# Kernel tuning notes

Hardware: AMD Instinct MI355X
Metric: run time of the kernel (lower is better)

Reference implementation:

```python
import math
import jax, jax.numpy as jnp
import numpy as np

EMBED_DIM = 128
NUM_HEADS = 2
B, N = 4096, 32  # batch of fully-connected ally graphs, N allies each (self-edges included)


def sparsemax(z, axis):
    """Sparsemax (Martins & Astudillo 2016) along `axis`."""
    K = z.shape[axis]
    z_sorted = -jnp.sort(-z, axis=axis)  # descending
    z_cumsum = jnp.cumsum(z_sorted, axis=axis)
    shape = [1] * z.ndim
    shape[axis] = K
    k = jnp.arange(1, K + 1, dtype=z.dtype).reshape(shape)
    support = (1.0 + k * z_sorted) > z_cumsum
    k_sup = jnp.sum(support.astype(z.dtype), axis=axis, keepdims=True)
    tau = (jnp.sum(jnp.where(support, z_sorted, 0.0), axis=axis, keepdims=True) - 1.0) / k_sup
    return jnp.maximum(z - tau, 0.0)


def setup_inputs() -> dict:
    key = jax.random.key(0)
    k1, k2, k3, k4 = jax.random.split(key, 4)
    D, H = EMBED_DIM, NUM_HEADS
    node_feature = jax.random.normal(k1, (B, N, D), dtype=jnp.float32)
    scale = 1.0 / math.sqrt(D)
    WK = jax.random.normal(k2, (D, H * D), dtype=jnp.float32) * scale
    WV = jax.random.normal(k3, (D, H * D), dtype=jnp.float32) * scale
    WQ = jax.random.normal(k4, (D, H * D), dtype=jnp.float32) * scale
    return {"node_feature": node_feature, "WK": WK, "WV": WV, "WQ": WQ}


def reference(node_feature, WK, WV, WQ):
    D, H = EMBED_DIM, NUM_HEADS
    x = node_feature  # [B, N, D]
    # per-node projections; Linear(D, H*D) reshaped to (H, D) as in torch .view
    k = (x @ WK).reshape(B, N, H, D)
    v = (x @ WV).reshape(B, N, H, D)
    q = (x @ WQ).reshape(B, N, H, D)
    # fully connected graph: node i attends over mailbox of all nodes j in same graph
    score = jnp.einsum("bihd,bjhd->bijh", q, k) / math.sqrt(D * H)  # [B, N(i), N(j), H]
    w = sparsemax(score, axis=2)  # sparsemax over neighbor (mailbox) dim
    out = jnp.einsum("bijh,bjhd->bihd", w, v)  # weighted reduction
    out = out.mean(axis=2)  # mean over heads -> [B, N, D]
    output = out.reshape(B * N, D)
    # weight padded to max_num_allies (= N here, so no extra padding needed)
    weight = w.reshape(B * N, N, H)
    return output, weight
```

## Files before the change

### kernel.cpp

```cpp
#include <hip/hip_runtime.h>
#include <hip/hip_bf16.h>


#define NG 4096

typedef short bf16x8 __attribute__((ext_vector_type(8)));
typedef short bf16x4 __attribute__((ext_vector_type(4)));
typedef float f32x4 __attribute__((ext_vector_type(4)));

__device__ inline short f2bf(float f) {
    __hip_bfloat16 h = __float2bfloat16(f);
    return __builtin_bit_cast(short, h);
}
__device__ inline float bf2f(short s) {
    return __builtin_bit_cast(float, ((unsigned)(unsigned short)s) << 16);
}
__device__ inline unsigned pack2(float a, float b) {
    return (unsigned)(unsigned short)f2bf(a) | ((unsigned)(unsigned short)f2bf(b) << 16);
}

#define TSWZ(node, col) ((((node) << 8)) + (((col) ^ (((node) & 7) << 3))))
#define VSWZ(row, col) ((((row) << 5) + (col)) ^ (((row) & 3) << 3))
#define XSWZ(node, col) (((node) << 7) + (((col) ^ (((node) & 7) << 3))))

__global__ void pack_mv_kernel(const float* __restrict__ WQ, const float* __restrict__ WK,
                               const float* __restrict__ WV,
                               short* __restrict__ pm, short* __restrict__ pv) {
    int gidx = blockIdx.x * 256 + threadIdx.x;
    if (gidx < 32768) {
        int idx  = gidx;
        int jj   = idx & 7;
        int lane = (idx >> 3) & 63;
        int s    = (idx >> 9) & 3;
        int mt   = (idx >> 11) & 15;
        int h    = mt >> 3;
        int a    = s * 32 + (lane >> 4) * 8 + jj;
        int bl   = (mt & 7) * 16 + (lane & 15);
        const float4* qa = (const float4*)(WQ + a * 256 + h * 128);
        const float4* kb = (const float4*)(WK + bl * 256 + h * 128);
        float acc = 0.f;
        #pragma unroll 8
        for (int c = 0; c < 32; ++c) {
            float4 q4 = qa[c], k4 = kb[c];
            acc += q4.x * k4.x + q4.y * k4.y + q4.z * k4.z + q4.w * k4.w;
        }
        pm[idx] = f2bf(acc * 0.0625f);
    } else {
        int idx  = gidx - 32768;
        int jj   = idx & 7;
        int lane = (idx >> 3) & 63;
        int s    = (idx >> 9) & 3;
        int t    = (idx >> 11) & 15;
        int krow = s * 32 + (lane >> 4) * 8 + jj;
        int col  = t * 16 + (lane & 15);
        pv[idx] = f2bf(WV[krow * 256 + col]);
    }
}

__global__ __launch_bounds__(256, 4)
void fused_attn_kernel(const float* __restrict__ x, const short* __restrict__ pm,
                       const short* __restrict__ pv, float* __restrict__ out,
                       float* __restrict__ wgt) {
    __shared__ char __align__(16) smem[32768];
    short* x_l  = (short*)smem;
    short* t_s  = (short*)smem;
    float* s_s  = (float*)smem;
    short* vT_s = (short*)(smem + 16384);

    int b    = blockIdx.x;
    int tid  = threadIdx.x;
    int lane = tid & 63;
    int wave = tid >> 6;
    int lrow = lane & 15;
    int quad = lane >> 4;

    const float* xg = x + (size_t)b * 4096;
    #pragma unroll
    for (int i = 0; i < 4; ++i) {
        int flat4 = i * 256 + tid;
        int node  = flat4 >> 5;
        int c4    = (flat4 & 31) * 4;
        float4 f  = *(const float4*)&xg[flat4 * 4];
        uint2 pk; pk.x = pack2(f.x, f.y); pk.y = pack2(f.z, f.w);
        *(uint2*)&x_l[XSWZ(node, c4)] = pk;
    }
    __syncthreads();

    bf16x8 xf[2][4];
    #pragma unroll
    for (int nt = 0; nt < 2; ++nt)
        #pragma unroll
        for (int s = 0; s < 4; ++s)
            xf[nt][s] = *(const bf16x8*)&x_l[XSWZ(nt * 16 + lrow, s * 32 + quad * 8)];
    __syncthreads();

    #pragma unroll
    for (int t = 0; t < 4; ++t) {
        int mt = wave * 4 + t;
        const short* pb = pm + (mt * 4) * 512 + lane * 8;
        bf16x8 wf[4];
        #pragma unroll
        for (int s = 0; s < 4; ++s) wf[s] = *(const bf16x8*)&pb[s * 512];
        f32x4 acc[2] = {{0.f,0.f,0.f,0.f},{0.f,0.f,0.f,0.f}};
        #pragma unroll
        for (int nt = 0; nt < 2; ++nt)
            #pragma unroll
            for (int s = 0; s < 4; ++s)
                acc[nt] = __builtin_amdgcn_mfma_f32_16x16x32_bf16(wf[s], xf[nt][s], acc[nt], 0, 0, 0);
        #pragma unroll
        for (int nt = 0; nt < 2; ++nt) {
            int node = nt * 16 + lrow;
            int addr = TSWZ(node, mt * 16 + quad * 4);
            uint2 pk; pk.x = pack2(acc[nt][0], acc[nt][1]); pk.y = pack2(acc[nt][2], acc[nt][3]);
            *(uint2*)&t_s[addr] = pk;
        }
    }
    #pragma unroll
    for (int t = 0; t < 4; ++t) {
        int ntv = wave * 4 + t;
        const short* pb = pv + (ntv * 4) * 512 + lane * 8;
        bf16x8 wf[4];
        #pragma unroll
        for (int s = 0; s < 4; ++s) wf[s] = *(const bf16x8*)&pb[s * 512];
        f32x4 acc[2] = {{0.f,0.f,0.f,0.f},{0.f,0.f,0.f,0.f}};
        #pragma unroll
        for (int mt = 0; mt < 2; ++mt)
            #pragma unroll
            for (int s = 0; s < 4; ++s)
                acc[mt] = __builtin_amdgcn_mfma_f32_16x16x32_bf16(xf[mt][s], wf[s], acc[mt], 0, 0, 0);
        #pragma unroll
        for (int mt = 0; mt < 2; ++mt) {
            int row = ntv * 16 + lrow;
            int idx = VSWZ(row, mt * 16 + quad * 4);
            uint2 pk; pk.x = pack2(acc[mt][0], acc[mt][1]); pk.y = pack2(acc[mt][2], acc[mt][3]);
            *(uint2*)&vT_s[idx] = pk;
        }
    }
    __syncthreads();

    f32x4 sacc[2];
    #pragma unroll
    for (int jt = 0; jt < 2; ++jt) {
        int h = wave >> 1, it = wave & 1;
        f32x4 acc = {0.f, 0.f, 0.f, 0.f};
        #pragma unroll
        for (int s = 0; s < 4; ++s) {
            int node = it * 16 + lrow;
            bf16x8 at = *(const bf16x8*)&t_s[TSWZ(node, h * 128 + s * 32 + quad * 8)];
            acc = __builtin_amdgcn_mfma_f32_16x16x32_bf16(at, xf[jt][s], acc, 0, 0, 0);
        }
        sacc[jt] = acc;
    }
    __syncthreads();

    #pragma unroll
    for (int jt = 0; jt < 2; ++jt)
        #pragma unroll
        for (int r = 0; r < 4; ++r)
            s_s[(wave * 16 + quad * 4 + r) * 36 + jt * 16 + lrow] = sacc[jt][r];

    {
        int j  = lane & 31;
        int hh = lane >> 5;
        #pragma unroll
        for (int ii = 0; ii < 8; ++ii) {
            int row = wave * 16 + hh * 8 + ii;
            const float* zr = &s_s[row * 36];
            float z[32];
            #pragma unroll
            for (int c = 0; c < 8; ++c) {
                float4 f = *(const float4*)&zr[c * 4];
                z[c*4] = f.x; z[c*4+1] = f.y; z[c*4+2] = f.z; z[c*4+3] = f.w;
            }
            float zj = zr[j];
            float c0 = 0.f, c1 = 0.f, s0 = 0.f, s1 = 0.f;
            #pragma unroll
            for (int l = 0; l < 32; l += 2) {
                float m0 = (z[l]     > zj) ? 1.f : 0.f;
                float m1 = (z[l + 1] > zj) ? 1.f : 0.f;
                c0 += m0;  s0 = __builtin_fmaf(m0, z[l],     s0);
                c1 += m1;  s1 = __builtin_fmaf(m1, z[l + 1], s1);
            }
            float rk  = c0 + c1 + 1.f;
            float cum = s0 + s1 + zj;
            float tc  = (cum - 1.f) / rk;
            #pragma unroll
            for (int m = 1; m <= 16; m <<= 1) tc = fmaxf(tc, __shfl_xor(tc, m, 32));
            float w = fmaxf(zj - tc, 0.f);
            ((short*)zr)[j] = f2bf(w);
        }
    }
    __syncthreads();

    #pragma unroll
    for (int tt = 0; tt < 4; ++tt) {
        int ti = wave * 4 + tt;
        int it = ti >> 3, dt = ti & 7;
        f32x4 acc = {0.f, 0.f, 0.f, 0.f};
        #pragma unroll
        for (int h = 0; h < 2; ++h) {
            int vrow = h * 128 + dt * 16 + lrow;
            bf16x8 aw = *(const bf16x8*)((short*)&s_s[(h * 32 + it * 16 + lrow) * 36] + quad * 8);
            bf16x8 bv = *(const bf16x8*)&vT_s[VSWZ(vrow, quad * 8)];
            acc = __builtin_amdgcn_mfma_f32_16x16x32_bf16(aw, bv, acc, 0, 0, 0);
        }
        #pragma unroll
        for (int r = 0; r < 4; ++r)
            out[((size_t)b * 32 + it * 16 + quad * 4 + r) * 128 + dt * 16 + lrow] = acc[r] * 0.5f;
    }
    {
        int i  = tid >> 3;
        int j2 = (tid & 7) * 4;
        bf16x4 a0 = *(const bf16x4*)((short*)&s_s[i * 36] + j2);
        bf16x4 a1 = *(const bf16x4*)((short*)&s_s[(32 + i) * 36] + j2);
        float4 o0, o1;
        o0.x = bf2f(a0[0]); o0.y = bf2f(a1[0]); o0.z = bf2f(a0[1]); o0.w = bf2f(a1[1]);
        o1.x = bf2f(a0[2]); o1.y = bf2f(a1[2]); o1.z = bf2f(a0[3]); o1.w = bf2f(a1[3]);
        float* wp = &wgt[((size_t)b * 32 + i) * 64 + j2 * 2];
        *(float4*)wp = o0;
        *(float4*)(wp + 4) = o1;
    }
}

extern "C" void kernel_launch(void* const* d_in, const int* in_sizes, int n_in,
                              void* d_out, int out_size, void* d_ws, size_t ws_size,
                              hipStream_t stream) {
    const float* x  = (const float*)d_in[0];
    const float* WK = (const float*)d_in[1];
    const float* WV = (const float*)d_in[2];
    const float* WQ = (const float*)d_in[3];
    float* out = (float*)d_out;
    float* wgt = out + (size_t)NG * 32 * 128;
    short* pm = (short*)d_ws;
    short* pv = pm + 32768;

    hipLaunchKernelGGL(pack_mv_kernel, dim3(256), dim3(256), 0, stream, WQ, WK, WV, pm, pv);
    hipLaunchKernelGGL(fused_attn_kernel, dim3(NG), dim3(256), 0, stream, x, pm, pv, out, wgt);
}
```

Measured before the change: 185.7 us.

## Compute sparsemax threshold in registers via shuffle bitonic sort and prefix scan

Replaces the old sparsemax path, which stored scores to LDS and ran an O(N^2) rank-and-sum loop per element, with an in-register bitonic sort of the 32 scores spread across 16 lanes times two values. A shuffle-based prefix sum then gives the cumulative sums, and a max-reduction over (cumsum-1)/k yields tau. This removes the LDS round trip for the scores and the quadratic compare work. In exchange it adds many cross-lane shuffles, and the bf16 weights are now written to a padded stride-40 short array.

```diff
diff --git a/kernel.cpp b/kernel.cpp
--- a/kernel.cpp
+++ b/kernel.cpp
@@ -64,7 +64,7 @@
     __shared__ char __align__(16) smem[32768];
     short* x_l  = (short*)smem;
     short* t_s  = (short*)smem;
-    float* s_s  = (float*)smem;
+    short* w_s  = (short*)smem;
     short* vT_s = (short*)(smem + 16384);
 
     int b    = blockIdx.x;
@@ -153,41 +153,75 @@
     }
     __syncthreads();
 
-    #pragma unroll
-    for (int jt = 0; jt < 2; ++jt)
-        #pragma unroll
-        for (int r = 0; r < 4; ++r)
-            s_s[(wave * 16 + quad * 4 + r) * 36 + jt * 16 + lrow] = sacc[jt][r];
-
     {
-        int j  = lane & 31;
-        int hh = lane >> 5;
-        #pragma unroll
-        for (int ii = 0; ii < 8; ++ii) {
-            int row = wave * 16 + hh * 8 + ii;
-            const float* zr = &s_s[row * 36];
-            float z[32];
-            #pragma unroll
-            for (int c = 0; c < 8; ++c) {
-                float4 f = *(const float4*)&zr[c * 4];
-                z[c*4] = f.x; z[c*4+1] = f.y; z[c*4+2] = f.z; z[c*4+3] = f.w;
-            }
-            float zj = zr[j];
-            float c0 = 0.f, c1 = 0.f, s0 = 0.f, s1 = 0.f;
-            #pragma unroll
-            for (int l = 0; l < 32; l += 2) {
-                float m0 = (z[l]     > zj) ? 1.f : 0.f;
-                float m1 = (z[l + 1] > zj) ? 1.f : 0.f;
-                c0 += m0;  s0 = __builtin_fmaf(m0, z[l],     s0);
-                c1 += m1;  s1 = __builtin_fmaf(m1, z[l + 1], s1);
-            }
-            float rk  = c0 + c1 + 1.f;
-            float cum = s0 + s1 + zj;
-            float tc  = (cum - 1.f) / rk;
-            #pragma unroll
-            for (int m = 1; m <= 16; m <<= 1) tc = fmaxf(tc, __shfl_xor(tc, m, 32));
-            float w = fmaxf(zj - tc, 0.f);
-            ((short*)zr)[j] = f2bf(w);
+        float rk0 = __builtin_amdgcn_rcpf((float)(lrow + 1));
+        float rk1 = __builtin_amdgcn_rcpf((float)(lrow + 17));
+        int b0 = (lrow >> 0) & 1, b1 = (lrow >> 1) & 1;
+        int b2 = (lrow >> 2) & 1, b3 = (lrow >> 3) & 1;
+        bool e01 = b0 == b1;
+        bool e12 = b1 == b2;
+        bool e02 = b0 == b2;
+        bool e23 = b2 == b3;
+        bool e13 = b1 == b3;
+        bool e03 = b0 == b3;
+        bool a0 = b0 == 0, a1 = b1 == 0, a2 = b2 == 0, a3 = b3 == 0;
+
+        #pragma unroll
+        for (int r = 0; r < 4; ++r) {
+            float v0 = sacc[0][r], v1 = sacc[1][r];
+            float p;
+            p = __shfl_xor(v0, 1, 16); v0 = e01 ? fmaxf(v0, p) : fminf(v0, p);
+            p = __shfl_xor(v1, 1, 16); v1 = e01 ? fmaxf(v1, p) : fminf(v1, p);
+            p = __shfl_xor(v0, 2, 16); v0 = e12 ? fmaxf(v0, p) : fminf(v0, p);
+            p = __shfl_xor(v1, 2, 16); v1 = e12 ? fmaxf(v1, p) : fminf(v1, p);
+            p = __shfl_xor(v0, 1, 16); v0 = e02 ? fmaxf(v0, p) : fminf(v0, p);
+            p = __shfl_xor(v1, 1, 16); v1 = e02 ? fmaxf(v1, p) : fminf(v1, p);
+            p = __shfl_xor(v0, 4, 16); v0 = e23 ? fmaxf(v0, p) : fminf(v0, p);
+            p = __shfl_xor(v1, 4, 16); v1 = e23 ? fmaxf(v1, p) : fminf(v1, p);
+            p = __shfl_xor(v0, 2, 16); v0 = e13 ? fmaxf(v0, p) : fminf(v0, p);
+            p = __shfl_xor(v1, 2, 16); v1 = e13 ? fmaxf(v1, p) : fminf(v1, p);
+            p = __shfl_xor(v0, 1, 16); v0 = e03 ? fmaxf(v0, p) : fminf(v0, p);
+            p = __shfl_xor(v1, 1, 16); v1 = e03 ? fmaxf(v1, p) : fminf(v1, p);
+            p = __shfl_xor(v0, 8, 16); v0 = a3 ? fmaxf(v0, p) : fminf(v0, p);
+            p = __shfl_xor(v1, 8, 16); v1 = a3 ? fminf(v1, p) : fmaxf(v1, p);
+            p = __shfl_xor(v0, 4, 16); v0 = a2 ? fmaxf(v0, p) : fminf(v0, p);
+            p = __shfl_xor(v1, 4, 16); v1 = a2 ? fminf(v1, p) : fmaxf(v1, p);
+            p = __shfl_xor(v0, 2, 16); v0 = a1 ? fmaxf(v0, p) : fminf(v0, p);
+            p = __shfl_xor(v1, 2, 16); v1 = a1 ? fminf(v1, p) : fmaxf(v1, p);
+            p = __shfl_xor(v0, 1, 16); v0 = a0 ? fmaxf(v0, p) : fminf(v0, p);
+            p = __shfl_xor(v1, 1, 16); v1 = a0 ? fminf(v1, p) : fmaxf(v1, p);
+            { float t = fmaxf(v0, v1); v1 = fminf(v0, v1); v0 = t; }
+            p = __shfl_xor(v0, 8, 16); v0 = a3 ? fmaxf(v0, p) : fminf(v0, p);
+            p = __shfl_xor(v1, 8, 16); v1 = a3 ? fmaxf(v1, p) : fminf(v1, p);
+            p = __shfl_xor(v0, 4, 16); v0 = a2 ? fmaxf(v0, p) : fminf(v0, p);
+            p = __shfl_xor(v1, 4, 16); v1 = a2 ? fmaxf(v1, p) : fminf(v1, p);
+            p = __shfl_xor(v0, 2, 16); v0 = a1 ? fmaxf(v0, p) : fminf(v0, p);
+            p = __shfl_xor(v1, 2, 16); v1 = a1 ? fmaxf(v1, p) : fminf(v1, p);
+            p = __shfl_xor(v0, 1, 16); v0 = a0 ? fmaxf(v0, p) : fminf(v0, p);
+            p = __shfl_xor(v1, 1, 16); v1 = a0 ? fmaxf(v1, p) : fminf(v1, p);
+            float c0 = v0;
+            p = __shfl_up(c0, 1, 16); c0 += (lrow >= 1) ? p : 0.f;
+            p = __shfl_up(c0, 2, 16); c0 += (lrow >= 2) ? p : 0.f;
+            p = __shfl_up(c0, 4, 16); c0 += (lrow >= 4) ? p : 0.f;
+            p = __shfl_up(c0, 8, 16); c0 += (lrow >= 8) ? p : 0.f;
+            float c1 = v1;
+            p = __shfl_up(c1, 1, 16); c1 += (lrow >= 1) ? p : 0.f;
+            p = __shfl_up(c1, 2, 16); c1 += (lrow >= 2) ? p : 0.f;
+            p = __shfl_up(c1, 4, 16); c1 += (lrow >= 4) ? p : 0.f;
+            p = __shfl_up(c1, 8, 16); c1 += (lrow >= 8) ? p : 0.f;
+            c1 += __shfl(c0, 15, 16);
+            float t0 = (c0 - 1.f) * rk0;
+            float t1 = (c1 - 1.f) * rk1;
+            float m = fmaxf(t0, t1);
+            m = fmaxf(m, __shfl_xor(m, 1, 16));
+            m = fmaxf(m, __shfl_xor(m, 2, 16));
+            m = fmaxf(m, __shfl_xor(m, 4, 16));
+            m = fmaxf(m, __shfl_xor(m, 8, 16));
+            int row = wave * 16 + quad * 4 + r;
+            float w0 = fmaxf(sacc[0][r] - m, 0.f);
+            float w1 = fmaxf(sacc[1][r] - m, 0.f);
+            w_s[row * 40 + lrow]      = f2bf(w0);
+            w_s[row * 40 + 16 + lrow] = f2bf(w1);
         }
     }
     __syncthreads();
@@ -200,7 +234,7 @@
         #pragma unroll
         for (int h = 0; h < 2; ++h) {
             int vrow = h * 128 + dt * 16 + lrow;
-            bf16x8 aw = *(const bf16x8*)((short*)&s_s[(h * 32 + it * 16 + lrow) * 36] + quad * 8);
+            bf16x8 aw = *(const bf16x8*)&w_s[(h * 32 + it * 16 + lrow) * 40 + quad * 8];
             bf16x8 bv = *(const bf16x8*)&vT_s[VSWZ(vrow, quad * 8)];
             acc = __builtin_amdgcn_mfma_f32_16x16x32_bf16(aw, bv, acc, 0, 0, 0);
         }
@@ -211,8 +245,8 @@
     {
         int i  = tid >> 3;
         int j2 = (tid & 7) * 4;
-        bf16x4 a0 = *(const bf16x4*)((short*)&s_s[i * 36] + j2);
-        bf16x4 a1 = *(const bf16x4*)((short*)&s_s[(32 + i) * 36] + j2);
+        bf16x4 a0 = *(const bf16x4*)&w_s[i * 40 + j2];
+        bf16x4 a1 = *(const bf16x4*)&w_s[(32 + i) * 40 + j2];
         float4 o0, o1;
         o0.x = bf2f(a0[0]); o0.y = bf2f(a1[0]); o0.z = bf2f(a0[1]); o0.w = bf2f(a1[1]);
         o1.x = bf2f(a0[2]); o1.y = bf2f(a1[2]); o1.z = bf2f(a0[3]); o1.w = bf2f(a1[3]);
```

Result: no change. 188.9 us (+1.7%).
